# Performance work log

Measured on AMD Instinct MI355X. Metric: run time of the kernel, lower is better.

The kernel has to match this reference:

```python
import jax, jax.numpy as jnp
import numpy as np

CONF_THRES = 0.25
IOU_THRES = 0.45
MAX_DET = 1000
MAX_WH = 4096.0   # class offset for per-class NMS (yolov5 trick)
TOPK = 2048       # pre-NMS candidate cap (fixed-shape stand-in for max_nms)


def _xywh2xyxy(b):
    cx, cy, w, h = b[..., 0], b[..., 1], b[..., 2], b[..., 3]
    return jnp.stack([cx - w * 0.5, cy - h * 0.5, cx + w * 0.5, cy + h * 0.5], axis=-1)


def _box_iou(a, b):
    # a, b: [K, 4] in xyxy -> [K, K] pairwise IoU
    lt = jnp.maximum(a[:, None, :2], b[None, :, :2])
    rb = jnp.minimum(a[:, None, 2:], b[None, :, 2:])
    wh = jnp.clip(rb - lt, 0.0)
    inter = wh[..., 0] * wh[..., 1]
    area_a = (a[:, 2] - a[:, 0]) * (a[:, 3] - a[:, 1])
    area_b = (b[:, 2] - b[:, 0]) * (b[:, 3] - b[:, 1])
    return inter / (area_a[:, None] + area_b[None, :] - inter + 1e-7)


def _nms_single(pred):
    # pred: [N, 5+C] = (cx, cy, w, h, obj, cls...)
    obj = pred[:, 4]
    cls_prob = pred[:, 5:]
    cls_conf = jnp.max(cls_prob, axis=-1)
    cls_id = jnp.argmax(cls_prob, axis=-1)
    score = obj * cls_conf                      # conf = obj_conf * cls_conf (best class)
    valid = (obj > CONF_THRES) & (score > CONF_THRES)
    score = jnp.where(valid, score, 0.0)
    boxes = _xywh2xyxy(pred[:, :4])

    # keep top-K candidates by confidence (sorted descending)
    tops, idx = jax.lax.top_k(score, TOPK)
    boxes_k = boxes[idx]                        # [K, 4]
    cls_k = cls_id[idx]                         # [K]
    val_k = tops > 0.0

    # per-class NMS via class offset
    shifted = boxes_k + (cls_k.astype(boxes_k.dtype) * MAX_WH)[:, None]
    iou = _box_iou(shifted, shifted)            # [K, K]

    j = jnp.arange(TOPK)

    def body(i, keep):
        # if box i survives, suppress lower-scored boxes with IoU > thresh
        sup = keep[i] & (iou[i] > IOU_THRES) & (j > i)
        return keep & ~sup

    keep = jax.lax.fori_loop(0, TOPK, body, val_k)

    # gather up to MAX_DET kept detections (already score-sorted)
    fs, fi = jax.lax.top_k(jnp.where(keep, tops, -1.0), MAX_DET)
    ok = fs > 0.0
    det_boxes = jnp.where(ok[:, None], boxes_k[fi], 0.0)
    det_score = jnp.where(ok, tops[fi], 0.0)
    det_cls = jnp.where(ok, cls_k[fi].astype(det_boxes.dtype), -1.0)
    # [MAX_DET, 6] = (x1, y1, x2, y2, conf, cls); padded rows have conf 0, cls -1
    return jnp.concatenate([det_boxes, det_score[:, None], det_cls[:, None]], axis=-1)


def setup_inputs() -> dict:
    key = jax.random.key(0)
    raw = jax.random.uniform(key, (16, 25200, 85), dtype=jnp.float32)
    xy = raw[..., 0:2] * 640.0            # centers within a 640x640 image
    wh = raw[..., 2:4] * 120.0 + 2.0      # box sizes in [2, 122]
    rest = raw[..., 4:]                   # obj + class probs in [0, 1)
    pred = jnp.concatenate([xy, wh, rest], axis=-1)
    return {"pred": pred}


def reference(pred):
    return jax.vmap(_nms_single)(pred)
```

## Files before the change

### kernel.cpp

```cpp
#include <hip/hip_runtime.h>
#include <stdint.h>

#pragma clang fp contract(off)

#define BB 16
#define NN 25200
#define ROW 85
#define NCLS 80
#define TK 2048
#define SORTN 4096
#define NBIN 4096
#define MAXDET 1000
#define CONF 0.25f
#define IOUT 0.45f
#define SROWS 64

typedef float fvec4 __attribute__((ext_vector_type(4)));

#define AS1 __attribute__((address_space(1)))
#define AS3 __attribute__((address_space(3)))

__global__ __launch_bounds__(128) void score_kernel(const float* __restrict__ pred,
                                                    float* __restrict__ scores,
                                                    uint8_t* __restrict__ cls,
                                                    unsigned int* __restrict__ hist) {
  __shared__ __align__(16) float srow[SROWS * ROW];
  const int tile = blockIdx.x;
  const int b = blockIdx.y;
  const int tid = threadIdx.x;
  const int lane = tid & 63;
  const int row0 = tile * SROWS;
  int nrows = NN - row0;
  if (nrows > SROWS) nrows = SROWS;
  const char* gsrc = (const char*)(pred + ((size_t)b * NN + row0) * ROW);
  const int nbytes = nrows * ROW * 4;
  for (int off = tid * 16; off < nbytes; off += 128 * 16) {
    __builtin_amdgcn_global_load_lds((AS1 void*)(gsrc + off),
                                     (AS3 void*)((char*)srow + (off - lane * 16)),
                                     16, 0, 0);
  }
  __builtin_amdgcn_s_waitcnt(0);
  __syncthreads();
  if (tid < nrows) {
    const int n = row0 + tid;
    const float* r = srow + tid * ROW;
    float obj = r[4];
    float best = r[5];
    int bid = 0;
#pragma unroll
    for (int c = 1; c < NCLS; ++c) {
      float p = r[5 + c];
      if (p > best) { best = p; bid = c; }
    }
    float score = obj * best;
    bool valid = (obj > CONF) && (score > CONF);
    float sout = valid ? score : 0.0f;
    scores[(size_t)b * NN + n] = sout;
    cls[(size_t)b * NN + n] = (uint8_t)bid;
    if (valid) {
      unsigned int u = __float_as_uint(sout);
      unsigned int bin = (u - 0x3E800001u) >> 12;
      if (bin > NBIN - 1) bin = NBIN - 1;
      atomicAdd(&hist[(size_t)b * NBIN + bin], 1u);
    }
  }
}

__global__ __launch_bounds__(256) void scan_kernel(const unsigned int* __restrict__ hist,
                                                   unsigned int* __restrict__ gsoff,
                                                   int* __restrict__ gP,
                                                   int* __restrict__ gtot) {
  const int b = blockIdx.x;
  const int t = threadIdx.x;
  const int w = t >> 6, lane = t & 63;
  const unsigned int* h = hist + (size_t)b * NBIN;
  unsigned int loc[16];
  int ssum = 0;
#pragma unroll
  for (int k = 0; k < 16; ++k) {
    loc[k] = h[NBIN - 1 - (16 * t + k)];
    ssum += (int)loc[k];
  }
  int v = ssum;
  for (int o = 1; o < 64; o <<= 1) { int u = __shfl_up(v, o); if (lane >= o) v += u; }
  __shared__ int sw[4];
  __shared__ int sfound;
  if (t == 0) sfound = 0;
  if (lane == 63) sw[w] = v;
  __syncthreads();
  int wbase = 0;
  for (int i = 0; i < w; ++i) wbase += sw[i];
  const int total = sw[0] + sw[1] + sw[2] + sw[3];
  int run = wbase + v - ssum;
#pragma unroll
  for (int k = 0; k < 16; ++k) {
    int bin = NBIN - 1 - (16 * t + k);
    gsoff[(size_t)b * NBIN + bin] = (unsigned int)run;
    int c = (int)loc[k];
    if (run < TK && run + c >= TK) {
      gP[b] = bin;
      gtot[b] = run + c;
      sfound = 1;
    }
    run += c;
  }
  __syncthreads();
  if (t == 0 && !sfound) { gP[b] = 0; gtot[b] = total; }
}

__global__ __launch_bounds__(1024) void scatter_kernel(const float* __restrict__ scores,
                                                       const unsigned int* __restrict__ gsoff,
                                                       const int* __restrict__ gP,
                                                       unsigned int* __restrict__ gcnt,
                                                       unsigned long long* __restrict__ gskey) {
  const int b = blockIdx.y;
  const int n = blockIdx.x * 1024 + threadIdx.x;
  if (n >= NN) return;
  const unsigned int P = (unsigned int)gP[b];
  unsigned int u = __float_as_uint(scores[(size_t)b * NN + n]);
  if (u > 0x3E800000u) {
    unsigned int bin = (u - 0x3E800001u) >> 12;
    if (bin > NBIN - 1) bin = NBIN - 1;
    if (bin >= P) {
      unsigned int pos = gsoff[(size_t)b * NBIN + bin] +
                         atomicAdd(&gcnt[(size_t)b * NBIN + bin], 1u);
      if (pos < SORTN)
        gskey[(size_t)b * SORTN + pos] = ((unsigned long long)u << 32) | (unsigned int)(~n);
    }
  }
}

__global__ __launch_bounds__(1024) void final_kernel(const float* __restrict__ pred,
                                                     const uint8_t* __restrict__ cls,
                                                     const unsigned int* __restrict__ gsoff,
                                                     const unsigned int* __restrict__ gcnt,
                                                     const unsigned long long* __restrict__ gskey,
                                                     const int* __restrict__ gtot,
                                                     float* __restrict__ out) {
  const int b = blockIdx.x;
  const int t = threadIdx.x;
  const int w = t >> 6;
  const int lane = t & 63;
  __shared__ unsigned long long skey[SORTN];
  __shared__ float sx1[TK], sy1[TK], sx2[TK], sy2[TK];
  __shared__ float stop[TK];
  __shared__ unsigned short scls[TK];
  __shared__ unsigned short cgrpL[TK];
  __shared__ unsigned char skp[TK];
  __shared__ int ccnt[NCLS];
  __shared__ int coffs[NCLS + 1];
  __shared__ int swsum[16];

  int total = gtot[b];
  int used = total < SORTN ? total : SORTN;
  int npos = total < TK ? total : TK;

  for (int i = t; i < used; i += 1024) skey[i] = gskey[(size_t)b * SORTN + i];
  for (int i = t; i < TK; i += 1024) {
    if (i >= npos) {
      sx1[i] = 0.f; sy1[i] = 0.f; sx2[i] = 0.f; sy2[i] = 0.f;
      stop[i] = 0.f;
      scls[i] = (unsigned short)0xFFFFu;
      skp[i] = 0;
    }
  }
  __syncthreads();

  for (int p = t; p < used; p += 1024) {
    unsigned long long k = skey[p];
    unsigned int u = (unsigned int)(k >> 32);
    unsigned int bin = (u - 0x3E800001u) >> 12;
    if (bin > NBIN - 1) bin = NBIN - 1;
    int base = (int)gsoff[(size_t)b * NBIN + bin];
    int cnt = (int)gcnt[(size_t)b * NBIN + bin];
    if (base + cnt > used) cnt = used - base;
    int rank = 0;
    for (int j = 0; j < cnt; ++j) rank += (skey[base + j] > k) ? 1 : 0;
    int q = base + rank;
    if (q < npos) {
      int idx = (int)(~(unsigned int)k);
      stop[q] = __uint_as_float(u);
      scls[q] = (unsigned short)cls[(size_t)b * NN + idx];
      skp[q] = 1;
      const float* rowp = pred + ((size_t)b * NN + idx) * ROW;
      float cx = rowp[0], cy = rowp[1], w2 = rowp[2], h2 = rowp[3];
      float hw = w2 * 0.5f, hh = h2 * 0.5f;
      sx1[q] = cx - hw; sy1[q] = cy - hh; sx2[q] = cx + hw; sy2[q] = cy + hh;
    }
  }
  __syncthreads();

#pragma unroll
  for (int k = 0; k < 5; ++k) {
    int c = w + 16 * k;
    int cnt = 0;
    for (int base2 = 0; base2 < TK; base2 += 64) {
      bool match = ((int)scls[base2 + lane] == c);
      cnt += (int)__popcll(__ballot(match));
    }
    if (lane == 0) ccnt[c] = cnt;
  }
  __syncthreads();
  if (t == 0) {
    int r2 = 0;
    for (int c = 0; c < NCLS; ++c) { coffs[c] = r2; r2 += ccnt[c]; }
    coffs[NCLS] = r2;
  }
  __syncthreads();
#pragma unroll
  for (int k = 0; k < 5; ++k) {
    int c = w + 16 * k;
    int run2 = coffs[c];
    for (int base2 = 0; base2 < TK; base2 += 64) {
      bool match = ((int)scls[base2 + lane] == c);
      unsigned long long bal = __ballot(match);
      int r3 = (int)__popcll(bal & ((1ull << lane) - 1ull));
      if (match) cgrpL[run2 + r3] = (unsigned short)(base2 + lane);
      run2 += (int)__popcll(bal);
    }
  }
  __syncthreads();

  for (int k = 0; k < 5; ++k) {
    int c = w + 16 * k;
    int start = coffs[c];
    int m = coffs[c + 1] - start;
    if (m <= 0) continue;
    int nq = (m + 63) >> 6;
    unsigned int km = 0;
    for (int q = 0; q < nq; ++q)
      if (lane + (q << 6) < m) km |= (1u << q);
    float b0x1 = 0.f, b0y1 = 0.f, b0x2 = 0.f, b0y2 = 0.f;
    if (lane < m) {
      int e0 = cgrpL[start + lane];
      b0x1 = sx1[e0]; b0y1 = sy1[e0]; b0x2 = sx2[e0]; b0y2 = sy2[e0];
    }
    for (int i = 0; i < m; ++i) {
      int q = i >> 6;
      unsigned int kmi = __shfl(km, i & 63);
      if (!((kmi >> q) & 1u)) continue;
      float ax1, ay1, ax2, ay2;
      if (q == 0) {
        ax1 = __shfl(b0x1, i); ay1 = __shfl(b0y1, i);
        ax2 = __shfl(b0x2, i); ay2 = __shfl(b0y2, i);
      } else {
        int ei = cgrpL[start + i];
        ax1 = sx1[ei]; ay1 = sy1[ei]; ax2 = sx2[ei]; ay2 = sy2[ei];
      }
      float aarea = (ax2 - ax1) * (ay2 - ay1);
      if ((km & 1u) && lane > i) {
        float ltx = fmaxf(ax1, b0x1), lty = fmaxf(ay1, b0y1);
        float rbx = fminf(ax2, b0x2), rby = fminf(ay2, b0y2);
        float iw = fmaxf(rbx - ltx, 0.0f);
        float ih = fmaxf(rby - lty, 0.0f);
        float inter = iw * ih;
        float barea = (b0x2 - b0x1) * (b0y2 - b0y1);
        float iou = inter / (aarea + barea - inter + 1e-7f);
        if (iou > IOUT) km &= ~1u;
      }
      for (int q2 = 1; q2 < nq; ++q2) {
        int j = lane + (q2 << 6);
        if (((km >> q2) & 1u) && j > i && j < m) {
          int ej = cgrpL[start + j];
          float jx1 = sx1[ej], jy1 = sy1[ej], jx2 = sx2[ej], jy2 = sy2[ej];
          float ltx = fmaxf(ax1, jx1), lty = fmaxf(ay1, jy1);
          float rbx = fminf(ax2, jx2), rby = fminf(ay2, jy2);
          float iw = fmaxf(rbx - ltx, 0.0f);
          float ih = fmaxf(rby - lty, 0.0f);
          float inter = iw * ih;
          float barea = (jx2 - jx1) * (jy2 - jy1);
          float iou = inter / (aarea + barea - inter + 1e-7f);
          if (iou > IOUT) km &= ~(1u << q2);
        }
      }
    }
    for (int q = 0; q < nq; ++q) {
      int j = lane + (q << 6);
      if (j < m) skp[cgrpL[start + j]] = (unsigned char)((km >> q) & 1u);
    }
  }
  __syncthreads();

  int kp0 = (int)skp[2 * t];
  int kp1 = (int)skp[2 * t + 1];
  int cnt2 = kp0 + kp1;
  int v2 = cnt2;
  for (int o = 1; o < 64; o <<= 1) { int u2 = __shfl_up(v2, o); if (lane >= o) v2 += u2; }
  if (lane == 63) swsum[w] = v2;
  __syncthreads();
  if (w == 0) {
    int x = (lane < 16) ? swsum[lane] : 0;
    for (int o = 1; o < 16; o <<= 1) { int u2 = __shfl_up(x, o); if (lane >= o) x += u2; }
    if (lane < 16) swsum[lane] = x;
  }
  __syncthreads();
  int r4 = (w ? swsum[w - 1] : 0) + v2 - cnt2;
  int K = swsum[15];
#pragma unroll
  for (int k = 0; k < 2; ++k) {
    int kp = (k == 0) ? kp0 : kp1;
    if (kp) {
      if (r4 < MAXDET) {
        int j = 2 * t + k;
        float* o = out + ((size_t)b * MAXDET + r4) * 6;
        o[0] = sx1[j]; o[1] = sy1[j]; o[2] = sx2[j]; o[3] = sy2[j];
        o[4] = stop[j];
        o[5] = (float)scls[j];
      }
      ++r4;
    }
  }
  int Kc = K < MAXDET ? K : MAXDET;
  for (int r2 = Kc + t; r2 < MAXDET; r2 += 1024) {
    float* o = out + ((size_t)b * MAXDET + r2) * 6;
    o[0] = 0.0f; o[1] = 0.0f; o[2] = 0.0f; o[3] = 0.0f; o[4] = 0.0f; o[5] = -1.0f;
  }
}

extern "C" void kernel_launch(void* const* d_in, const int* in_sizes, int n_in,
                              void* d_out, int out_size, void* d_ws, size_t ws_size,
                              hipStream_t stream) {
  const float* pred = (const float*)d_in[0];
  float* out = (float*)d_out;

  char* ws = (char*)d_ws;
  size_t off = 0;
  float*              scores = (float*)(ws + off);              off += (size_t)BB * NN * 4;
  uint8_t*            cls    = (uint8_t*)(ws + off);            off += (size_t)BB * NN;
  off = (off + 255) & ~(size_t)255;
  unsigned int*       hist   = (unsigned int*)(ws + off);       off += (size_t)BB * NBIN * 4;
  unsigned int*       gcnt   = (unsigned int*)(ws + off);       off += (size_t)BB * NBIN * 4;
  unsigned int*       gsoff  = (unsigned int*)(ws + off);       off += (size_t)BB * NBIN * 4;
  unsigned long long* gskey  = (unsigned long long*)(ws + off); off += (size_t)BB * SORTN * 8;
  int*                gP     = (int*)(ws + off);                off += (size_t)BB * 4;
  int*                gtot   = (int*)(ws + off);                off += (size_t)BB * 4;
  (void)ws_size; (void)in_sizes; (void)n_in; (void)out_size;

  hipMemsetAsync(hist, 0, (size_t)BB * NBIN * 4 * 2, stream);
  score_kernel<<<dim3((NN + SROWS - 1) / SROWS, BB), 128, 0, stream>>>(pred, scores, cls, hist);
  scan_kernel<<<BB, 256, 0, stream>>>(hist, gsoff, gP, gtot);
  scatter_kernel<<<dim3((NN + 1023) / 1024, BB), 1024, 0, stream>>>(scores, gsoff, gP, gcnt, gskey);
  final_kernel<<<BB, 1024, 0, stream>>>(pred, cls, gsoff, gcnt, gskey, gtot, out);
}
```

Measured before the change: 278.5 us.

## Fuse histogram, scan, and scatter into the per-batch final kernel using LDS

Removes the global histogram memset, scan kernel and scatter kernel. The single per-batch block now builds the score histogram in LDS, scans it, and scatters the candidate keys into shared memory before the existing rank, class-grouping and NMS stages. The aim is to cut launch count and global atomic and memory traffic. In exchange, only 16 blocks re-read the 25200 scores per batch twice, so the histogram and scatter phases run with little parallelism. Class ids are also cached in registers for the grouping ballots, which adds register pressure.

```diff
diff --git a/kernel.cpp b/kernel.cpp
--- a/kernel.cpp
+++ b/kernel.cpp
@@ -14,6 +14,7 @@
 #define CONF 0.25f
 #define IOUT 0.45f
 #define SROWS 64
+#define STH 0x3E800000u
 
 typedef float fvec4 __attribute__((ext_vector_type(4)));
 
@@ -22,8 +23,7 @@
 
 __global__ __launch_bounds__(128) void score_kernel(const float* __restrict__ pred,
                                                     float* __restrict__ scores,
-                                                    uint8_t* __restrict__ cls,
-                                                    unsigned int* __restrict__ hist) {
+                                                    uint8_t* __restrict__ cls) {
   __shared__ __align__(16) float srow[SROWS * ROW];
   const int tile = blockIdx.x;
   const int b = blockIdx.y;
@@ -54,93 +54,21 @@
     }
     float score = obj * best;
     bool valid = (obj > CONF) && (score > CONF);
-    float sout = valid ? score : 0.0f;
-    scores[(size_t)b * NN + n] = sout;
+    scores[(size_t)b * NN + n] = valid ? score : 0.0f;
     cls[(size_t)b * NN + n] = (uint8_t)bid;
-    if (valid) {
-      unsigned int u = __float_as_uint(sout);
-      unsigned int bin = (u - 0x3E800001u) >> 12;
-      if (bin > NBIN - 1) bin = NBIN - 1;
-      atomicAdd(&hist[(size_t)b * NBIN + bin], 1u);
-    }
   }
 }
 
-__global__ __launch_bounds__(256) void scan_kernel(const unsigned int* __restrict__ hist,
-                                                   unsigned int* __restrict__ gsoff,
-                                                   int* __restrict__ gP,
-                                                   int* __restrict__ gtot) {
-  const int b = blockIdx.x;
-  const int t = threadIdx.x;
-  const int w = t >> 6, lane = t & 63;
-  const unsigned int* h = hist + (size_t)b * NBIN;
-  unsigned int loc[16];
-  int ssum = 0;
-#pragma unroll
-  for (int k = 0; k < 16; ++k) {
-    loc[k] = h[NBIN - 1 - (16 * t + k)];
-    ssum += (int)loc[k];
-  }
-  int v = ssum;
-  for (int o = 1; o < 64; o <<= 1) { int u = __shfl_up(v, o); if (lane >= o) v += u; }
-  __shared__ int sw[4];
-  __shared__ int sfound;
-  if (t == 0) sfound = 0;
-  if (lane == 63) sw[w] = v;
-  __syncthreads();
-  int wbase = 0;
-  for (int i = 0; i < w; ++i) wbase += sw[i];
-  const int total = sw[0] + sw[1] + sw[2] + sw[3];
-  int run = wbase + v - ssum;
-#pragma unroll
-  for (int k = 0; k < 16; ++k) {
-    int bin = NBIN - 1 - (16 * t + k);
-    gsoff[(size_t)b * NBIN + bin] = (unsigned int)run;
-    int c = (int)loc[k];
-    if (run < TK && run + c >= TK) {
-      gP[b] = bin;
-      gtot[b] = run + c;
-      sfound = 1;
-    }
-    run += c;
-  }
-  __syncthreads();
-  if (t == 0 && !sfound) { gP[b] = 0; gtot[b] = total; }
-}
-
-__global__ __launch_bounds__(1024) void scatter_kernel(const float* __restrict__ scores,
-                                                       const unsigned int* __restrict__ gsoff,
-                                                       const int* __restrict__ gP,
-                                                       unsigned int* __restrict__ gcnt,
-                                                       unsigned long long* __restrict__ gskey) {
-  const int b = blockIdx.y;
-  const int n = blockIdx.x * 1024 + threadIdx.x;
-  if (n >= NN) return;
-  const unsigned int P = (unsigned int)gP[b];
-  unsigned int u = __float_as_uint(scores[(size_t)b * NN + n]);
-  if (u > 0x3E800000u) {
-    unsigned int bin = (u - 0x3E800001u) >> 12;
-    if (bin > NBIN - 1) bin = NBIN - 1;
-    if (bin >= P) {
-      unsigned int pos = gsoff[(size_t)b * NBIN + bin] +
-                         atomicAdd(&gcnt[(size_t)b * NBIN + bin], 1u);
-      if (pos < SORTN)
-        gskey[(size_t)b * SORTN + pos] = ((unsigned long long)u << 32) | (unsigned int)(~n);
-    }
-  }
-}
-
-__global__ __launch_bounds__(1024) void final_kernel(const float* __restrict__ pred,
-                                                     const uint8_t* __restrict__ cls,
-                                                     const unsigned int* __restrict__ gsoff,
-                                                     const unsigned int* __restrict__ gcnt,
-                                                     const unsigned long long* __restrict__ gskey,
-                                                     const int* __restrict__ gtot,
-                                                     float* __restrict__ out) {
+__global__ __launch_bounds__(1024) void mega_kernel(const float* __restrict__ pred,
+                                                    const float* __restrict__ scores,
+                                                    const uint8_t* __restrict__ cls,
+                                                    float* __restrict__ out) {
   const int b = blockIdx.x;
   const int t = threadIdx.x;
   const int w = t >> 6;
   const int lane = t & 63;
+  __shared__ unsigned int hist[NBIN];
+  __shared__ unsigned int soff[NBIN];
   __shared__ unsigned long long skey[SORTN];
   __shared__ float sx1[TK], sy1[TK], sx2[TK], sy2[TK];
   __shared__ float stop[TK];
@@ -150,29 +78,87 @@
   __shared__ int ccnt[NCLS];
   __shared__ int coffs[NCLS + 1];
   __shared__ int swsum[16];
-
-  int total = gtot[b];
-  int used = total < SORTN ? total : SORTN;
-  int npos = total < TK ? total : TK;
-
-  for (int i = t; i < used; i += 1024) skey[i] = gskey[(size_t)b * SORTN + i];
-  for (int i = t; i < TK; i += 1024) {
-    if (i >= npos) {
-      sx1[i] = 0.f; sy1[i] = 0.f; sx2[i] = 0.f; sy2[i] = 0.f;
-      stop[i] = 0.f;
-      scls[i] = (unsigned short)0xFFFFu;
-      skp[i] = 0;
-    }
+  __shared__ int sP, sTot, sfound;
+
+  const unsigned int* su = (const unsigned int*)(scores + (size_t)b * NN);
+
+  for (int i = t; i < NBIN; i += 1024) hist[i] = 0u;
+  if (t == 0) sfound = 0;
+  __syncthreads();
+
+  for (int n = t; n < NN; n += 1024) {
+    unsigned int u = su[n];
+    if (u > STH) {
+      unsigned int bin = (u - (STH + 1u)) >> 12;
+      if (bin > NBIN - 1) bin = NBIN - 1;
+      atomicAdd(&hist[bin], 1u);
+    }
+  }
+  __syncthreads();
+
+  int loc[4];
+  int ssum = 0;
+#pragma unroll
+  for (int k = 0; k < 4; ++k) {
+    loc[k] = (int)hist[NBIN - 1 - (4 * t + k)];
+    ssum += loc[k];
+  }
+  int v = ssum;
+  for (int o = 1; o < 64; o <<= 1) { int uu = __shfl_up(v, o); if (lane >= o) v += uu; }
+  if (lane == 63) swsum[w] = v;
+  __syncthreads();
+  if (w == 0) {
+    int x = (lane < 16) ? swsum[lane] : 0;
+    for (int o = 1; o < 16; o <<= 1) { int uu = __shfl_up(x, o); if (lane >= o) x += uu; }
+    if (lane < 16) swsum[lane] = x;
+  }
+  __syncthreads();
+  const int total = swsum[15];
+  int run = (w ? swsum[w - 1] : 0) + (v - ssum);
+#pragma unroll
+  for (int k = 0; k < 4; ++k) {
+    int bin = NBIN - 1 - (4 * t + k);
+    soff[bin] = (unsigned int)run;
+    if (run < TK && run + loc[k] >= TK) {
+      sP = bin; sTot = run + loc[k]; sfound = 1;
+    }
+    run += loc[k];
+  }
+  __syncthreads();
+  if (t == 0 && !sfound) { sP = 0; sTot = total; }
+  __syncthreads();
+  const int P = sP;
+  const int tot = sTot;
+  const int used = tot < SORTN ? tot : SORTN;
+  const int npos = tot < TK ? tot : TK;
+
+  for (int n = t; n < NN; n += 1024) {
+    unsigned int u = su[n];
+    if (u > STH) {
+      unsigned int bin = (u - (STH + 1u)) >> 12;
+      if (bin > NBIN - 1) bin = NBIN - 1;
+      if ((int)bin >= P) {
+        unsigned int pos = atomicAdd(&soff[bin], 1u);
+        if (pos < SORTN)
+          skey[pos] = ((unsigned long long)u << 32) | (unsigned int)(~n);
+      }
+    }
+  }
+  for (int i = npos + t; i < TK; i += 1024) {
+    sx1[i] = 0.f; sy1[i] = 0.f; sx2[i] = 0.f; sy2[i] = 0.f;
+    stop[i] = 0.f;
+    scls[i] = (unsigned short)0xFFFFu;
+    skp[i] = 0;
   }
   __syncthreads();
 
   for (int p = t; p < used; p += 1024) {
     unsigned long long k = skey[p];
     unsigned int u = (unsigned int)(k >> 32);
-    unsigned int bin = (u - 0x3E800001u) >> 12;
+    unsigned int bin = (u - (STH + 1u)) >> 12;
     if (bin > NBIN - 1) bin = NBIN - 1;
-    int base = (int)gsoff[(size_t)b * NBIN + bin];
-    int cnt = (int)gcnt[(size_t)b * NBIN + bin];
+    int cnt = (int)hist[bin];
+    int base = (int)soff[bin] - cnt;
     if (base + cnt > used) cnt = used - base;
     int rank = 0;
     for (int j = 0; j < cnt; ++j) rank += (skey[base + j] > k) ? 1 : 0;
@@ -190,14 +176,16 @@
   }
   __syncthreads();
 
+  int myv[32];
+#pragma unroll
+  for (int ch = 0; ch < 32; ++ch) myv[ch] = (int)scls[ch * 64 + lane];
 #pragma unroll
   for (int k = 0; k < 5; ++k) {
     int c = w + 16 * k;
     int cnt = 0;
-    for (int base2 = 0; base2 < TK; base2 += 64) {
-      bool match = ((int)scls[base2 + lane] == c);
-      cnt += (int)__popcll(__ballot(match));
-    }
+#pragma unroll
+    for (int ch = 0; ch < 32; ++ch)
+      cnt += (int)__popcll(__ballot(myv[ch] == c));
     if (lane == 0) ccnt[c] = cnt;
   }
   __syncthreads();
@@ -211,11 +199,12 @@
   for (int k = 0; k < 5; ++k) {
     int c = w + 16 * k;
     int run2 = coffs[c];
-    for (int base2 = 0; base2 < TK; base2 += 64) {
-      bool match = ((int)scls[base2 + lane] == c);
+#pragma unroll
+    for (int ch = 0; ch < 32; ++ch) {
+      bool match = (myv[ch] == c);
       unsigned long long bal = __ballot(match);
       int r3 = (int)__popcll(bal & ((1ull << lane) - 1ull));
-      if (match) cgrpL[run2 + r3] = (unsigned short)(base2 + lane);
+      if (match) cgrpL[run2 + r3] = (unsigned short)(ch * 64 + lane);
       run2 += (int)__popcll(bal);
     }
   }
@@ -325,20 +314,10 @@
 
   char* ws = (char*)d_ws;
   size_t off = 0;
-  float*              scores = (float*)(ws + off);              off += (size_t)BB * NN * 4;
-  uint8_t*            cls    = (uint8_t*)(ws + off);            off += (size_t)BB * NN;
-  off = (off + 255) & ~(size_t)255;
-  unsigned int*       hist   = (unsigned int*)(ws + off);       off += (size_t)BB * NBIN * 4;
-  unsigned int*       gcnt   = (unsigned int*)(ws + off);       off += (size_t)BB * NBIN * 4;
-  unsigned int*       gsoff  = (unsigned int*)(ws + off);       off += (size_t)BB * NBIN * 4;
-  unsigned long long* gskey  = (unsigned long long*)(ws + off); off += (size_t)BB * SORTN * 8;
-  int*                gP     = (int*)(ws + off);                off += (size_t)BB * 4;
-  int*                gtot   = (int*)(ws + off);                off += (size_t)BB * 4;
+  float*   scores = (float*)(ws + off);   off += (size_t)BB * NN * 4;
+  uint8_t* cls    = (uint8_t*)(ws + off); off += (size_t)BB * NN;
   (void)ws_size; (void)in_sizes; (void)n_in; (void)out_size;
 
-  hipMemsetAsync(hist, 0, (size_t)BB * NBIN * 4 * 2, stream);
-  score_kernel<<<dim3((NN + SROWS - 1) / SROWS, BB), 128, 0, stream>>>(pred, scores, cls, hist);
-  scan_kernel<<<BB, 256, 0, stream>>>(hist, gsoff, gP, gtot);
-  scatter_kernel<<<dim3((NN + 1023) / 1024, BB), 1024, 0, stream>>>(scores, gsoff, gP, gcnt, gskey);
-  final_kernel<<<BB, 1024, 0, stream>>>(pred, cls, gsoff, gcnt, gskey, gtot, out);
+  score_kernel<<<dim3((NN + SROWS - 1) / SROWS, BB), 128, 0, stream>>>(pred, scores, cls);
+  mega_kernel<<<BB, 1024, 0, stream>>>(pred, scores, cls, out);
 }
```

Result: no change. 283.2 us (+1.7%).

## Split monolithic final kernel into emit, per-class NMS, and output kernels

Applied to the files above, without the earlier changes.

Replaces the single 16-block final kernel with three kernels. The first ranks and emits the sorted candidates using 4 blocks per batch. The second runs NMS with one 64-thread block per (class, batch) pair, 1280 blocks in all. The third compacts the kept boxes into the output. The goal is to spread the serial per-class NMS loop, previously run by 16 waves per block across 16 blocks, over many CUs. The cost is global-memory round trips for the intermediates and two extra launches. Clearing gcnt also moves from the memset into scan_kernel.

```diff
diff --git a/kernel.cpp b/kernel.cpp
--- a/kernel.cpp
+++ b/kernel.cpp
@@ -14,6 +14,7 @@
 #define CONF 0.25f
 #define IOUT 0.45f
 #define SROWS 64
+#define STH 0x3E800000u
 
 typedef float fvec4 __attribute__((ext_vector_type(4)));
 
@@ -59,7 +60,7 @@
     cls[(size_t)b * NN + n] = (uint8_t)bid;
     if (valid) {
       unsigned int u = __float_as_uint(sout);
-      unsigned int bin = (u - 0x3E800001u) >> 12;
+      unsigned int bin = (u - (STH + 1u)) >> 12;
       if (bin > NBIN - 1) bin = NBIN - 1;
       atomicAdd(&hist[(size_t)b * NBIN + bin], 1u);
     }
@@ -68,11 +69,13 @@
 
 __global__ __launch_bounds__(256) void scan_kernel(const unsigned int* __restrict__ hist,
                                                    unsigned int* __restrict__ gsoff,
+                                                   unsigned int* __restrict__ gcnt,
                                                    int* __restrict__ gP,
                                                    int* __restrict__ gtot) {
   const int b = blockIdx.x;
   const int t = threadIdx.x;
   const int w = t >> 6, lane = t & 63;
+  for (int i = t; i < NBIN; i += 256) gcnt[(size_t)b * NBIN + i] = 0u;
   const unsigned int* h = hist + (size_t)b * NBIN;
   unsigned int loc[16];
   int ssum = 0;
@@ -118,8 +121,8 @@
   if (n >= NN) return;
   const unsigned int P = (unsigned int)gP[b];
   unsigned int u = __float_as_uint(scores[(size_t)b * NN + n]);
-  if (u > 0x3E800000u) {
-    unsigned int bin = (u - 0x3E800001u) >> 12;
+  if (u > STH) {
+    unsigned int bin = (u - (STH + 1u)) >> 12;
     if (bin > NBIN - 1) bin = NBIN - 1;
     if (bin >= P) {
       unsigned int pos = gsoff[(size_t)b * NBIN + bin] +
@@ -130,188 +133,148 @@
   }
 }
 
-__global__ __launch_bounds__(1024) void final_kernel(const float* __restrict__ pred,
-                                                     const uint8_t* __restrict__ cls,
-                                                     const unsigned int* __restrict__ gsoff,
-                                                     const unsigned int* __restrict__ gcnt,
-                                                     const unsigned long long* __restrict__ gskey,
-                                                     const int* __restrict__ gtot,
-                                                     float* __restrict__ out) {
-  const int b = blockIdx.x;
-  const int t = threadIdx.x;
-  const int w = t >> 6;
-  const int lane = t & 63;
-  __shared__ unsigned long long skey[SORTN];
-  __shared__ float sx1[TK], sy1[TK], sx2[TK], sy2[TK];
-  __shared__ float stop[TK];
-  __shared__ unsigned short scls[TK];
-  __shared__ unsigned short cgrpL[TK];
-  __shared__ unsigned char skp[TK];
-  __shared__ int ccnt[NCLS];
-  __shared__ int coffs[NCLS + 1];
-  __shared__ int swsum[16];
-
-  int total = gtot[b];
-  int used = total < SORTN ? total : SORTN;
-  int npos = total < TK ? total : TK;
-
-  for (int i = t; i < used; i += 1024) skey[i] = gskey[(size_t)b * SORTN + i];
-  for (int i = t; i < TK; i += 1024) {
-    if (i >= npos) {
-      sx1[i] = 0.f; sy1[i] = 0.f; sx2[i] = 0.f; sy2[i] = 0.f;
-      stop[i] = 0.f;
-      scls[i] = (unsigned short)0xFFFFu;
-      skp[i] = 0;
-    }
-  }
-  __syncthreads();
-
-  for (int p = t; p < used; p += 1024) {
-    unsigned long long k = skey[p];
+__global__ __launch_bounds__(1024) void emit_kernel(const float* __restrict__ pred,
+                                                    const uint8_t* __restrict__ cls,
+                                                    const unsigned int* __restrict__ gsoff,
+                                                    const unsigned int* __restrict__ gcnt,
+                                                    const unsigned long long* __restrict__ gskey,
+                                                    const int* __restrict__ gtot,
+                                                    float* __restrict__ gtops,
+                                                    fvec4* __restrict__ gbox,
+                                                    int* __restrict__ gcls) {
+  const int b = blockIdx.y;
+  const int stride = gridDim.x * 1024;
+  const int tot = gtot[b];
+  const int used = tot < SORTN ? tot : SORTN;
+  const int npos = tot < TK ? tot : TK;
+  for (int ip = npos + blockIdx.x * 1024 + threadIdx.x; ip < TK; ip += stride) {
+    gtops[(size_t)b * TK + ip] = 0.0f;
+    gcls[(size_t)b * TK + ip] = 0xFFFF;
+    fvec4 z; z[0] = 0.f; z[1] = 0.f; z[2] = 0.f; z[3] = 0.f;
+    gbox[(size_t)b * TK + ip] = z;
+  }
+  for (int pp = blockIdx.x * 1024 + threadIdx.x; pp < used; pp += stride) {
+    unsigned long long k = gskey[(size_t)b * SORTN + pp];
     unsigned int u = (unsigned int)(k >> 32);
-    unsigned int bin = (u - 0x3E800001u) >> 12;
+    unsigned int bin = (u - (STH + 1u)) >> 12;
     if (bin > NBIN - 1) bin = NBIN - 1;
     int base = (int)gsoff[(size_t)b * NBIN + bin];
     int cnt = (int)gcnt[(size_t)b * NBIN + bin];
     if (base + cnt > used) cnt = used - base;
+    const unsigned long long* seg = gskey + (size_t)b * SORTN + base;
     int rank = 0;
-    for (int j = 0; j < cnt; ++j) rank += (skey[base + j] > k) ? 1 : 0;
+    for (int j = 0; j < cnt; ++j) rank += (seg[j] > k) ? 1 : 0;
     int q = base + rank;
     if (q < npos) {
       int idx = (int)(~(unsigned int)k);
-      stop[q] = __uint_as_float(u);
-      scls[q] = (unsigned short)cls[(size_t)b * NN + idx];
-      skp[q] = 1;
+      gtops[(size_t)b * TK + q] = __uint_as_float(u);
+      gcls[(size_t)b * TK + q] = (int)cls[(size_t)b * NN + idx];
       const float* rowp = pred + ((size_t)b * NN + idx) * ROW;
       float cx = rowp[0], cy = rowp[1], w2 = rowp[2], h2 = rowp[3];
       float hw = w2 * 0.5f, hh = h2 * 0.5f;
-      sx1[q] = cx - hw; sy1[q] = cy - hh; sx2[q] = cx + hw; sy2[q] = cy + hh;
-    }
-  }
-  __syncthreads();
-
-#pragma unroll
-  for (int k = 0; k < 5; ++k) {
-    int c = w + 16 * k;
-    int cnt = 0;
-    for (int base2 = 0; base2 < TK; base2 += 64) {
-      bool match = ((int)scls[base2 + lane] == c);
-      cnt += (int)__popcll(__ballot(match));
-    }
-    if (lane == 0) ccnt[c] = cnt;
-  }
-  __syncthreads();
-  if (t == 0) {
-    int r2 = 0;
-    for (int c = 0; c < NCLS; ++c) { coffs[c] = r2; r2 += ccnt[c]; }
-    coffs[NCLS] = r2;
-  }
-  __syncthreads();
-#pragma unroll
-  for (int k = 0; k < 5; ++k) {
-    int c = w + 16 * k;
-    int run2 = coffs[c];
-    for (int base2 = 0; base2 < TK; base2 += 64) {
-      bool match = ((int)scls[base2 + lane] == c);
-      unsigned long long bal = __ballot(match);
-      int r3 = (int)__popcll(bal & ((1ull << lane) - 1ull));
-      if (match) cgrpL[run2 + r3] = (unsigned short)(base2 + lane);
-      run2 += (int)__popcll(bal);
-    }
-  }
-  __syncthreads();
-
-  for (int k = 0; k < 5; ++k) {
-    int c = w + 16 * k;
-    int start = coffs[c];
-    int m = coffs[c + 1] - start;
-    if (m <= 0) continue;
-    int nq = (m + 63) >> 6;
-    unsigned int km = 0;
-    for (int q = 0; q < nq; ++q)
-      if (lane + (q << 6) < m) km |= (1u << q);
-    float b0x1 = 0.f, b0y1 = 0.f, b0x2 = 0.f, b0y2 = 0.f;
-    if (lane < m) {
-      int e0 = cgrpL[start + lane];
-      b0x1 = sx1[e0]; b0y1 = sy1[e0]; b0x2 = sx2[e0]; b0y2 = sy2[e0];
-    }
-    for (int i = 0; i < m; ++i) {
-      int q = i >> 6;
-      unsigned int kmi = __shfl(km, i & 63);
-      if (!((kmi >> q) & 1u)) continue;
-      float ax1, ay1, ax2, ay2;
-      if (q == 0) {
-        ax1 = __shfl(b0x1, i); ay1 = __shfl(b0y1, i);
-        ax2 = __shfl(b0x2, i); ay2 = __shfl(b0y2, i);
-      } else {
-        int ei = cgrpL[start + i];
-        ax1 = sx1[ei]; ay1 = sy1[ei]; ax2 = sx2[ei]; ay2 = sy2[ei];
+      fvec4 bb4;
+      bb4[0] = cx - hw; bb4[1] = cy - hh; bb4[2] = cx + hw; bb4[3] = cy + hh;
+      gbox[(size_t)b * TK + q] = bb4;
+    }
+  }
+}
+
+__global__ __launch_bounds__(64) void nms_kernel(const float* __restrict__ gtops,
+                                                 const fvec4* __restrict__ gbox,
+                                                 const int* __restrict__ gcls,
+                                                 int* __restrict__ keep) {
+  const int c = blockIdx.x;
+  const int b = blockIdx.y;
+  const int lane = threadIdx.x;
+  __shared__ float sx1[TK], sy1[TK], sx2[TK], sy2[TK];
+  __shared__ unsigned short spos[TK];
+  __shared__ unsigned char skp[TK];
+
+  int m = 0;
+  for (int base = 0; base < TK; base += 64) {
+    int j = base + lane;
+    bool match = (gcls[(size_t)b * TK + j] == c);
+    unsigned long long bal = __ballot(match);
+    int mp = m + __popcll(bal & ((1ull << lane) - 1ull));
+    if (match) {
+      spos[mp] = (unsigned short)j;
+      fvec4 bx = gbox[(size_t)b * TK + j];
+      sx1[mp] = bx[0]; sy1[mp] = bx[1]; sx2[mp] = bx[2]; sy2[mp] = bx[3];
+      skp[mp] = (gtops[(size_t)b * TK + j] > 0.0f) ? 1 : 0;
+    }
+    m += (int)__popcll(bal);
+  }
+  __syncthreads();
+
+  for (int i = 0; i < m; ++i) {
+    __syncthreads();
+    if (!skp[i]) continue;
+    float ax1 = sx1[i], ay1 = sy1[i], ax2 = sx2[i], ay2 = sy2[i];
+    float aarea = (ax2 - ax1) * (ay2 - ay1);
+    for (int j = i + 1 + lane; j < m; j += 64) {
+      float bx1 = sx1[j], by1 = sy1[j], bx2 = sx2[j], by2 = sy2[j];
+      float ltx = fmaxf(ax1, bx1), lty = fmaxf(ay1, by1);
+      float rbx = fminf(ax2, bx2), rby = fminf(ay2, by2);
+      float iw = fmaxf(rbx - ltx, 0.0f);
+      float ih = fmaxf(rby - lty, 0.0f);
+      float inter = iw * ih;
+      float barea = (bx2 - bx1) * (by2 - by1);
+      float iou = inter / (aarea + barea - inter + 1e-7f);
+      if (iou > IOUT) skp[j] = 0;
+    }
+  }
+  __syncthreads();
+
+  for (int i = lane; i < m; i += 64) {
+    keep[(size_t)b * TK + spos[i]] = skp[i];
+  }
+}
+
+__global__ __launch_bounds__(256) void out_kernel(const float* __restrict__ gtops,
+                                                  const fvec4* __restrict__ gbox,
+                                                  const int* __restrict__ gcls,
+                                                  const int* __restrict__ keep,
+                                                  const int* __restrict__ gtot,
+                                                  float* __restrict__ out) {
+  int b = blockIdx.x;
+  int t = threadIdx.x;
+  __shared__ int scnt[256];
+  int npos = gtot[b];
+  if (npos > TK) npos = TK;
+  const int CH = TK / 256;
+  int base = t * CH;
+  int kp[CH];
+  int cnt = 0;
+  for (int k = 0; k < CH; ++k) {
+    int j = base + k;
+    kp[k] = (j < npos) ? keep[(size_t)b * TK + j] : 0;
+    cnt += kp[k];
+  }
+  scnt[t] = cnt;
+  __syncthreads();
+  for (int off = 1; off < 256; off <<= 1) {
+    int v = (t >= off) ? scnt[t - off] : 0;
+    __syncthreads();
+    scnt[t] += v;
+    __syncthreads();
+  }
+  int r = scnt[t] - cnt;
+  int K = scnt[255];
+  for (int k = 0; k < CH; ++k) {
+    if (kp[k]) {
+      if (r < MAXDET) {
+        int j = base + k;
+        float* o = out + ((size_t)b * MAXDET + r) * 6;
+        fvec4 bx = gbox[(size_t)b * TK + j];
+        o[0] = bx[0]; o[1] = bx[1]; o[2] = bx[2]; o[3] = bx[3];
+        o[4] = gtops[(size_t)b * TK + j];
+        o[5] = (float)gcls[(size_t)b * TK + j];
       }
-      float aarea = (ax2 - ax1) * (ay2 - ay1);
-      if ((km & 1u) && lane > i) {
-        float ltx = fmaxf(ax1, b0x1), lty = fmaxf(ay1, b0y1);
-        float rbx = fminf(ax2, b0x2), rby = fminf(ay2, b0y2);
-        float iw = fmaxf(rbx - ltx, 0.0f);
-        float ih = fmaxf(rby - lty, 0.0f);
-        float inter = iw * ih;
-        float barea = (b0x2 - b0x1) * (b0y2 - b0y1);
-        float iou = inter / (aarea + barea - inter + 1e-7f);
-        if (iou > IOUT) km &= ~1u;
-      }
-      for (int q2 = 1; q2 < nq; ++q2) {
-        int j = lane + (q2 << 6);
-        if (((km >> q2) & 1u) && j > i && j < m) {
-          int ej = cgrpL[start + j];
-          float jx1 = sx1[ej], jy1 = sy1[ej], jx2 = sx2[ej], jy2 = sy2[ej];
-          float ltx = fmaxf(ax1, jx1), lty = fmaxf(ay1, jy1);
-          float rbx = fminf(ax2, jx2), rby = fminf(ay2, jy2);
-          float iw = fmaxf(rbx - ltx, 0.0f);
-          float ih = fmaxf(rby - lty, 0.0f);
-          float inter = iw * ih;
-          float barea = (jx2 - jx1) * (jy2 - jy1);
-          float iou = inter / (aarea + barea - inter + 1e-7f);
-          if (iou > IOUT) km &= ~(1u << q2);
-        }
-      }
-    }
-    for (int q = 0; q < nq; ++q) {
-      int j = lane + (q << 6);
-      if (j < m) skp[cgrpL[start + j]] = (unsigned char)((km >> q) & 1u);
-    }
-  }
-  __syncthreads();
-
-  int kp0 = (int)skp[2 * t];
-  int kp1 = (int)skp[2 * t + 1];
-  int cnt2 = kp0 + kp1;
-  int v2 = cnt2;
-  for (int o = 1; o < 64; o <<= 1) { int u2 = __shfl_up(v2, o); if (lane >= o) v2 += u2; }
-  if (lane == 63) swsum[w] = v2;
-  __syncthreads();
-  if (w == 0) {
-    int x = (lane < 16) ? swsum[lane] : 0;
-    for (int o = 1; o < 16; o <<= 1) { int u2 = __shfl_up(x, o); if (lane >= o) x += u2; }
-    if (lane < 16) swsum[lane] = x;
-  }
-  __syncthreads();
-  int r4 = (w ? swsum[w - 1] : 0) + v2 - cnt2;
-  int K = swsum[15];
-#pragma unroll
-  for (int k = 0; k < 2; ++k) {
-    int kp = (k == 0) ? kp0 : kp1;
-    if (kp) {
-      if (r4 < MAXDET) {
-        int j = 2 * t + k;
-        float* o = out + ((size_t)b * MAXDET + r4) * 6;
-        o[0] = sx1[j]; o[1] = sy1[j]; o[2] = sx2[j]; o[3] = sy2[j];
-        o[4] = stop[j];
-        o[5] = (float)scls[j];
-      }
-      ++r4;
+      ++r;
     }
   }
   int Kc = K < MAXDET ? K : MAXDET;
-  for (int r2 = Kc + t; r2 < MAXDET; r2 += 1024) {
+  for (int r2 = Kc + t; r2 < MAXDET; r2 += 256) {
     float* o = out + ((size_t)b * MAXDET + r2) * 6;
     o[0] = 0.0f; o[1] = 0.0f; o[2] = 0.0f; o[3] = 0.0f; o[4] = 0.0f; o[5] = -1.0f;
   }
@@ -332,13 +295,20 @@
   unsigned int*       gcnt   = (unsigned int*)(ws + off);       off += (size_t)BB * NBIN * 4;
   unsigned int*       gsoff  = (unsigned int*)(ws + off);       off += (size_t)BB * NBIN * 4;
   unsigned long long* gskey  = (unsigned long long*)(ws + off); off += (size_t)BB * SORTN * 8;
+  float*              gtops  = (float*)(ws + off);              off += (size_t)BB * TK * 4;
+  fvec4*              gbox   = (fvec4*)(ws + off);              off += (size_t)BB * TK * 16;
+  int*                gcls   = (int*)(ws + off);                off += (size_t)BB * TK * 4;
+  int*                keep   = (int*)(ws + off);                off += (size_t)BB * TK * 4;
   int*                gP     = (int*)(ws + off);                off += (size_t)BB * 4;
   int*                gtot   = (int*)(ws + off);                off += (size_t)BB * 4;
   (void)ws_size; (void)in_sizes; (void)n_in; (void)out_size;
 
-  hipMemsetAsync(hist, 0, (size_t)BB * NBIN * 4 * 2, stream);
+  hipMemsetAsync(hist, 0, (size_t)BB * NBIN * 4, stream);
   score_kernel<<<dim3((NN + SROWS - 1) / SROWS, BB), 128, 0, stream>>>(pred, scores, cls, hist);
-  scan_kernel<<<BB, 256, 0, stream>>>(hist, gsoff, gP, gtot);
+  scan_kernel<<<BB, 256, 0, stream>>>(hist, gsoff, gcnt, gP, gtot);
   scatter_kernel<<<dim3((NN + 1023) / 1024, BB), 1024, 0, stream>>>(scores, gsoff, gP, gcnt, gskey);
-  final_kernel<<<BB, 1024, 0, stream>>>(pred, cls, gsoff, gcnt, gskey, gtot, out);
-}
+  emit_kernel<<<dim3(SORTN / 1024, BB), 1024, 0, stream>>>(pred, cls, gsoff, gcnt, gskey, gtot,
+                                                           gtops, gbox, gcls);
+  nms_kernel<<<dim3(NCLS, BB), 64, 0, stream>>>(gtops, gbox, gcls, keep);
+  out_kernel<<<BB, 256, 0, stream>>>(gtops, gbox, gcls, keep, gtot, out);
+}
```

Result: faster. 260.5 us (-6.5%).
